# Performance work log

Measured on AMD Instinct MI355X. Metric: run time of the kernel, lower is better.

## Reference

```python
import jax, jax.numpy as jnp
import numpy as np

N, E, F_IN, H, G, A, OUT = 50000, 800000, 128, 256, 64, 8, 1


def _lin(k, fi, fo):
    s = 1.0 / np.sqrt(fi)
    kw, kb = jax.random.split(k)
    W = jax.random.uniform(kw, (fi, fo), jnp.float32, -s, s)
    b = jax.random.uniform(kb, (fo,), jnp.float32, -s, s)
    return W, b


def setup_inputs() -> dict:
    key = jax.random.key(0)
    ks = jax.random.split(key, 12)
    x = jax.random.normal(ks[0], (N, F_IN), jnp.float32)
    edge_index = jax.random.randint(ks[1], (2, E), 0, N, dtype=jnp.int64)
    batch = jnp.sort(jax.random.randint(ks[2], (N,), 0, G, dtype=jnp.int64))
    graph_attr = jax.random.normal(ks[3], (G, A), jnp.float32)
    W1, b1 = _lin(ks[4], F_IN, H)
    W2, b2 = _lin(ks[5], H, H)
    W3, b3 = _lin(ks[6], H, H)
    fcW1, fcb1 = _lin(ks[7], H + A, H)
    fcW2, fcb2 = _lin(ks[8], H, OUT)
    ones = jnp.ones((H,), jnp.float32)
    zeros = jnp.zeros((H,), jnp.float32)
    return dict(x=x, graph_attr=graph_attr, edge_index=edge_index, batch=batch,
                W1=W1, b1=b1, W2=W2, b2=b2, W3=W3, b3=b3,
                g1=ones, be1=zeros, g2=ones, be2=zeros, g3=ones, be3=zeros,
                fcW1=fcW1, fcb1=fcb1, fcW2=fcW2, fcb2=fcb2)


def gcn_conv(x, W, b, src, dst, n):
    # PyG GCNConv: add self-loops, symmetric normalization, xW then scatter-add
    xw = x @ W  # [N, H]
    loop = jnp.arange(n)
    src2 = jnp.concatenate([src, loop])
    dst2 = jnp.concatenate([dst, loop])
    deg = jnp.zeros((n,), xw.dtype).at[dst2].add(1.0)
    dinv = jnp.where(deg > 0, jax.lax.rsqrt(deg), 0.0)
    norm = dinv[src2] * dinv[dst2]  # [E+N]
    out = jnp.zeros((n, xw.shape[1]), xw.dtype).at[dst2].add(xw[src2] * norm[:, None])
    return out + b


def layer_norm(x, g, b, eps=1e-5):
    m = x.mean(-1, keepdims=True)
    v = ((x - m) ** 2).mean(-1, keepdims=True)
    return (x - m) * jax.lax.rsqrt(v + eps) * g + b


def reference(x, graph_attr, edge_index, batch,
              W1, b1, W2, b2, W3, b3,
              g1, be1, g2, be2, g3, be3,
              fcW1, fcb1, fcW2, fcb2):
    src, dst = edge_index[0], edge_index[1]
    h = jax.nn.relu(layer_norm(gcn_conv(x, W1, b1, src, dst, N), g1, be1))
    h = jax.nn.relu(layer_norm(gcn_conv(h, W2, b2, src, dst, N), g2, be2))
    h = jax.nn.relu(layer_norm(gcn_conv(h, W3, b3, src, dst, N), g3, be3))
    # global mean pool over graph ids
    sums = jax.ops.segment_sum(h, batch, num_segments=G)
    cnts = jax.ops.segment_sum(jnp.ones((N,), h.dtype), batch, num_segments=G)
    pooled = sums / jnp.maximum(cnts, 1.0)[:, None]  # [G, H]
    z = jnp.concatenate([pooled, graph_attr.reshape(-1, A)], axis=1)
    z = jax.nn.relu(z @ fcW1 + fcb1)
    return z @ fcW2 + fcb2  # [G, OUT]
```

## Files before the change

### kernel.cpp

```cpp
#include <hip/hip_runtime.h>
#include <hip/hip_bf16.h>

#define N_NODES 50000
#define N_EDGES 800000
#define F_IN    128
#define H_DIM   256
#define G_NUM   64
#define A_DIM   8

typedef __attribute__((ext_vector_type(8))) short short8v;
typedef __attribute__((ext_vector_type(4))) float float4v;
typedef __attribute__((ext_vector_type(2))) float float2v;

__device__ __forceinline__ float b2f(unsigned short u) {
    return __uint_as_float(((unsigned int)u) << 16);
}
__device__ __forceinline__ unsigned short f2b(float v) {
    return __hip_bfloat16_raw(__float2bfloat16(v)).x;
}
__device__ __forceinline__ unsigned char f2fp8(float v) {
    return (unsigned char)(__builtin_amdgcn_cvt_pk_fp8_f32(v, v, 0, false) & 0xff);
}
__device__ __forceinline__ unsigned int pack2(float a, float b) {
    return (unsigned int)f2b(a) | ((unsigned int)f2b(b) << 16);
}
__device__ __forceinline__ void accadd16(float2v* a, uint4 v) {
    a[0] += __builtin_amdgcn_cvt_pk_f32_fp8((int)v.x, false);
    a[1] += __builtin_amdgcn_cvt_pk_f32_fp8((int)v.x, true);
    a[2] += __builtin_amdgcn_cvt_pk_f32_fp8((int)v.y, false);
    a[3] += __builtin_amdgcn_cvt_pk_f32_fp8((int)v.y, true);
    a[4] += __builtin_amdgcn_cvt_pk_f32_fp8((int)v.z, false);
    a[5] += __builtin_amdgcn_cvt_pk_f32_fp8((int)v.z, true);
    a[6] += __builtin_amdgcn_cvt_pk_f32_fp8((int)v.w, false);
    a[7] += __builtin_amdgcn_cvt_pk_f32_fp8((int)v.w, true);
}

#define SK 40


__global__ __launch_bounds__(512) void fuseA_kernel(const int* __restrict__ dst,
                                                    int* __restrict__ indeg,
                                                    unsigned short* __restrict__ eloc,
                                                    const float* __restrict__ x,
                                                    const float* __restrict__ W1,
                                                    unsigned short* __restrict__ Hb,
                                                    const float* __restrict__ W2,
                                                    unsigned short* __restrict__ Wt2,
                                                    const float* __restrict__ W3,
                                                    unsigned short* __restrict__ Wt3) {
    const int EB = (N_EDGES + 511) / 512;
    const int GB = (N_NODES + 127) / 128;
    int b = blockIdx.x, t = threadIdx.x;
    if (b < EB) {
        int i = b * 512 + t;
        if (i < N_EDGES)
            eloc[i] = (unsigned short)atomicAdd(&indeg[dst[i]], 1);
        return;
    }
    b -= EB;
    if (b < GB) {
        __shared__ unsigned short As[128][SK];
        __shared__ unsigned short Bs[256][SK];
        int wave = t >> 6, lane = t & 63;
        int wm0 = (wave & 1) * 64, wn0 = (wave >> 1) * 64;
        int bm = b * 128;
        int l15 = lane & 15, lq = lane >> 4;
        float4v acc[4][4];
        #pragma unroll
        for (int i = 0; i < 4; i++)
            #pragma unroll
            for (int j = 0; j < 4; j++)
                acc[i][j] = (float4v){0.f, 0.f, 0.f, 0.f};

        for (int k0 = 0; k0 < F_IN; k0 += 32) {
            {
                int row = t >> 2, koff = (t & 3) * 8;
                short8v tmp = (short8v){0,0,0,0,0,0,0,0};
                if (bm + row < N_NODES) {
                    const float* xp = x + (size_t)(bm + row) * F_IN + k0 + koff;
                    float4 a0 = *(const float4*)xp;
                    float4 a1 = *(const float4*)(xp + 4);
                    tmp[0] = (short)f2b(a0.x); tmp[1] = (short)f2b(a0.y);
                    tmp[2] = (short)f2b(a0.z); tmp[3] = (short)f2b(a0.w);
                    tmp[4] = (short)f2b(a1.x); tmp[5] = (short)f2b(a1.y);
                    tmp[6] = (short)f2b(a1.z); tmp[7] = (short)f2b(a1.w);
                }
                *(short8v*)&As[row][koff] = tmp;
            }
            #pragma unroll
            for (int h = 0; h < 2; h++) {
                int c = t + h * 512;
                int n = c >> 2, koff = (c & 3) * 8;
                short8v tmp;
                #pragma unroll
                for (int kk = 0; kk < 8; kk++)
                    tmp[kk] = (short)f2b(W1[(size_t)(k0 + koff + kk) * H_DIM + n]);
                *(short8v*)&Bs[n][koff] = tmp;
            }
            __syncthreads();
            short8v af[4], bf[4];
            #pragma unroll
            for (int i = 0; i < 4; i++) {
                af[i] = *(const short8v*)&As[wm0 + i * 16 + l15][lq * 8];
                bf[i] = *(const short8v*)&Bs[wn0 + i * 16 + l15][lq * 8];
            }
            #pragma unroll
            for (int i = 0; i < 4; i++)
                #pragma unroll
                for (int j = 0; j < 4; j++)
                    acc[i][j] = __builtin_amdgcn_mfma_f32_16x16x32_bf16(af[i], bf[j], acc[i][j], 0, 0, 0);
            __syncthreads();
        }
        #pragma unroll
        for (int i = 0; i < 4; i++) {
            #pragma unroll
            for (int r = 0; r < 4; r++) {
                int row = bm + wm0 + i * 16 + lq * 4 + r;
                if (row < N_NODES) {
                    #pragma unroll
                    for (int j = 0; j < 4; j++) {
                        int col = wn0 + j * 16 + l15;
                        Hb[(size_t)row * H_DIM + col] = f2b(acc[i][j][r]);
                    }
                }
            }
        }
        return;
    }
    b -= GB;
    int i = b * 512 + t;
    if (i < H_DIM * H_DIM) {
        int k = i >> 8, n = i & 255;
        Wt2[(size_t)n * H_DIM + k] = f2b(W2[i]);
    } else if (i < 2 * H_DIM * H_DIM) {
        int j = i - H_DIM * H_DIM;
        int k = j >> 8, n = j & 255;
        Wt3[(size_t)n * H_DIM + k] = f2b(W3[j]);
    }
}


__global__ __launch_bounds__(256) void scan1_kernel(const int* __restrict__ in,
                                                    int* __restrict__ out,
                                                    int* __restrict__ bsum,
                                                    float* __restrict__ dinv, int n) {
    __shared__ int tile[256];
    int b = blockIdx.x, t = threadIdx.x, i = b * 256 + t;
    int v = (i < n) ? in[i] : 0;
    if (i < n) dinv[i] = rsqrtf((float)v + 1.0f);
    tile[t] = v;
    __syncthreads();
    #pragma unroll
    for (int o = 1; o < 256; o <<= 1) {
        int add = (t >= o) ? tile[t - o] : 0;
        __syncthreads();
        tile[t] += add;
        __syncthreads();
    }
    if (i < n) out[i] = tile[t] - v;
    if (t == 255) bsum[b] = tile[255];
}

__global__ __launch_bounds__(256) void scan2_kernel(int* __restrict__ bsum, int nb,
                                                    const int* __restrict__ batch,
                                                    int* __restrict__ gstart,
                                                    float* __restrict__ pooled) {
    __shared__ int tile[256];
    int t = threadIdx.x;
    int v = (t < nb) ? bsum[t] : 0;
    tile[t] = v;
    __syncthreads();
    #pragma unroll
    for (int o = 1; o < 256; o <<= 1) {
        int add = (t >= o) ? tile[t - o] : 0;
        __syncthreads();
        tile[t] += add;
        __syncthreads();
    }
    if (t < nb) bsum[t] = tile[t] - v;
    if (t <= G_NUM) {
        int lo = 0, hi = N_NODES;
        while (lo < hi) {
            int mid = (lo + hi) >> 1;
            if (batch[mid] < t) lo = mid + 1; else hi = mid;
        }
        gstart[t] = lo;
    }
    for (int i = t; i < G_NUM * H_DIM; i += 256) pooled[i] = 0.f;
}

__global__ __launch_bounds__(256) void scan3_kernel(int* __restrict__ out,
                                                    const int* __restrict__ bsum, int n) {
    int i = blockIdx.x * blockDim.x + threadIdx.x;
    if (i < n) out[i] = out[i] + bsum[i >> 8];
    if (i == 0) out[n] = N_EDGES;
}


__global__ __launch_bounds__(512) void fuseB_kernel(const int* __restrict__ src,
                                                    const int* __restrict__ dst,
                                                    const unsigned short* __restrict__ eloc,
                                                    const int* __restrict__ rowptr,
                                                    unsigned short* __restrict__ csr_src,
                                                    const uint4* __restrict__ Hb4,
                                                    const float* __restrict__ dinv,
                                                    uint2* __restrict__ P8) {
    const int PB = (N_EDGES + 511) / 512;
    int b = blockIdx.x, t = threadIdx.x;
    if (b < PB) {
        int i = b * 512 + t;
        if (i < N_EDGES) {
            int d = dst[i];
            csr_src[rowptr[d] + (int)eloc[i]] = (unsigned short)src[i];
        }
        return;
    }
    int i = (b - PB) * 512 + t;
    if (i < N_NODES * (H_DIM / 8)) {
        float dv = dinv[i >> 5];
        uint4 hv = Hb4[i];
        float f0 = b2f((unsigned short)(hv.x & 0xffffu)) * dv;
        float f1 = b2f((unsigned short)(hv.x >> 16)) * dv;
        float f2 = b2f((unsigned short)(hv.y & 0xffffu)) * dv;
        float f3 = b2f((unsigned short)(hv.y >> 16)) * dv;
        float f4 = b2f((unsigned short)(hv.z & 0xffffu)) * dv;
        float f5 = b2f((unsigned short)(hv.z >> 16)) * dv;
        float f6 = b2f((unsigned short)(hv.w & 0xffffu)) * dv;
        float f7 = b2f((unsigned short)(hv.w >> 16)) * dv;
        unsigned int lo = (unsigned int)__builtin_amdgcn_cvt_pk_fp8_f32(f0, f1, 0, false);
        lo = (unsigned int)__builtin_amdgcn_cvt_pk_fp8_f32(f2, f3, (int)lo, true);
        unsigned int hi = (unsigned int)__builtin_amdgcn_cvt_pk_fp8_f32(f4, f5, 0, false);
        hi = (unsigned int)__builtin_amdgcn_cvt_pk_fp8_f32(f6, f7, (int)hi, true);
        P8[i] = make_uint2(lo, hi);
    }
}


__device__ __forceinline__ void gemm_body_f8(const unsigned short* __restrict__ A,
                                             const unsigned short* __restrict__ Bt,
                                             unsigned char* __restrict__ C8,
                                             const float* __restrict__ dinv,
                                             int M, int K, int bm) {
    __shared__ unsigned short As[128][SK];
    __shared__ unsigned short Bs[256][SK];
    int t = threadIdx.x;
    int wave = t >> 6, lane = t & 63;
    int wm0 = (wave & 1) * 64, wn0 = (wave >> 1) * 64;
    int l15 = lane & 15, lq = lane >> 4;
    float4v acc[4][4];
    #pragma unroll
    for (int i = 0; i < 4; i++)
        #pragma unroll
        for (int j = 0; j < 4; j++)
            acc[i][j] = (float4v){0.f, 0.f, 0.f, 0.f};

    for (int k0 = 0; k0 < K; k0 += 32) {
        {
            int row = t >> 2, koff = (t & 3) * 8;
            uint4 va = make_uint4(0u, 0u, 0u, 0u);
            if (bm + row < M)
                va = *(const uint4*)(A + (size_t)(bm + row) * K + k0 + koff);
            *(uint4*)&As[row][koff] = va;
        }
        #pragma unroll
        for (int h = 0; h < 2; h++) {
            int c = t + h * 512;
            int row = c >> 2, koff = (c & 3) * 8;
            uint4 vb = *(const uint4*)(Bt + (size_t)row * K + k0 + koff);
            *(uint4*)&Bs[row][koff] = vb;
        }
        __syncthreads();
        short8v af[4], bf[4];
        #pragma unroll
        for (int i = 0; i < 4; i++) {
            af[i] = *(const short8v*)&As[wm0 + i * 16 + l15][lq * 8];
            bf[i] = *(const short8v*)&Bs[wn0 + i * 16 + l15][lq * 8];
        }
        #pragma unroll
        for (int i = 0; i < 4; i++)
            #pragma unroll
            for (int j = 0; j < 4; j++)
                acc[i][j] = __builtin_amdgcn_mfma_f32_16x16x32_bf16(af[i], bf[j], acc[i][j], 0, 0, 0);
        __syncthreads();
    }
    #pragma unroll
    for (int i = 0; i < 4; i++) {
        #pragma unroll
        for (int r = 0; r < 4; r++) {
            int row = bm + wm0 + i * 16 + lq * 4 + r;
            if (row < M) {
                float dv = dinv[row];
                #pragma unroll
                for (int j = 0; j < 4; j++) {
                    int col = wn0 + j * 16 + l15;
                    C8[(size_t)row * H_DIM + col] = f2fp8(dv * acc[i][j][r]);
                }
            }
        }
    }
}

__global__ __launch_bounds__(512) void gemm_f8(const unsigned short* __restrict__ A,
                                               const unsigned short* __restrict__ Bt,
                                               unsigned char* __restrict__ C8,
                                               const float* __restrict__ dinv,
                                               int M, int K) {
    gemm_body_f8(A, Bt, C8, dinv, M, K, blockIdx.x * 128);
}


template<int F, bool DO_LN>
__global__ __launch_bounds__(256) void gather_ns(const unsigned char* __restrict__ xw,
                                                 unsigned short* __restrict__ out,
                                                 const int* __restrict__ rowptr,
                                                 const unsigned short* __restrict__ csr_src,
                                                 const float* __restrict__ dinv,
                                                 const float* __restrict__ bias,
                                                 const float* __restrict__ gamma,
                                                 const float* __restrict__ beta) {
    constexpr int BPL = F / 16;
    constexpr int NF2 = BPL / 2;
    int lane = threadIdx.x & 63;
    int wave = threadIdx.x >> 6;
    int p = lane & 15;
    int gbase = lane & 48;
    int node = blockIdx.x * 16 + wave * 4 + (lane >> 4);
    int beg = rowptr[node];
    int deg = rowptr[node + 1] - beg;
    const unsigned char* xp = xw + (size_t)p * BPL;

    float2v acc2[NF2];
    #pragma unroll
    for (int k = 0; k < NF2; k++) acc2[k] = (float2v){0.f, 0.f};

    {
        uint4 v = *(const uint4*)(xp + (size_t)node * F);
        accadd16(acc2, v);
    }

    for (int b0 = 0; b0 < deg; b0 += 16) {
        int m = deg - b0; if (m > 16) m = 16;
        int sv = (p < m) ? (int)csr_src[beg + b0 + p] : 0;
        int j = 0;
        for (; j + 4 <= m; j += 4) {
            int s0 = __shfl(sv, gbase | j, 64);
            int s1 = __shfl(sv, gbase | (j + 1), 64);
            int s2 = __shfl(sv, gbase | (j + 2), 64);
            int s3 = __shfl(sv, gbase | (j + 3), 64);
            uint4 v0 = *(const uint4*)(xp + (size_t)s0 * F);
            uint4 v1 = *(const uint4*)(xp + (size_t)s1 * F);
            uint4 v2 = *(const uint4*)(xp + (size_t)s2 * F);
            uint4 v3 = *(const uint4*)(xp + (size_t)s3 * F);
            accadd16(acc2, v0); accadd16(acc2, v1);
            accadd16(acc2, v2); accadd16(acc2, v3);
        }
        for (; j < m; ++j) {
            int s0 = __shfl(sv, gbase | j, 64);
            uint4 v0 = *(const uint4*)(xp + (size_t)s0 * F);
            accadd16(acc2, v0);
        }
    }

    float d = dinv[node];
    float v[BPL];
    #pragma unroll
    for (int k = 0; k < NF2; k++) { v[2 * k] = d * acc2[k].x; v[2 * k + 1] = d * acc2[k].y; }

    if constexpr (DO_LN) {
        #pragma unroll
        for (int q = 0; q < BPL / 4; q++) {
            float4 bi = ((const float4*)bias)[p * (BPL / 4) + q];
            v[q * 4 + 0] += bi.x; v[q * 4 + 1] += bi.y;
            v[q * 4 + 2] += bi.z; v[q * 4 + 3] += bi.w;
        }
        float s = 0.f, ss = 0.f;
        #pragma unroll
        for (int k = 0; k < BPL; k++) { s += v[k]; ss += v[k] * v[k]; }
        #pragma unroll
        for (int o = 1; o < 16; o <<= 1) {
            s  += __shfl_xor(s, o, 64);
            ss += __shfl_xor(ss, o, 64);
        }
        float mn = s * (1.f / F);
        float var = ss * (1.f / F) - mn * mn;
        float rstd = rsqrtf(var + 1e-5f);
        #pragma unroll
        for (int q = 0; q < BPL / 4; q++) {
            float4 ga = ((const float4*)gamma)[p * (BPL / 4) + q];
            float4 be = ((const float4*)beta)[p * (BPL / 4) + q];
            v[q * 4 + 0] = fmaxf((v[q * 4 + 0] - mn) * rstd * ga.x + be.x, 0.f);
            v[q * 4 + 1] = fmaxf((v[q * 4 + 1] - mn) * rstd * ga.y + be.y, 0.f);
            v[q * 4 + 2] = fmaxf((v[q * 4 + 2] - mn) * rstd * ga.z + be.z, 0.f);
            v[q * 4 + 3] = fmaxf((v[q * 4 + 3] - mn) * rstd * ga.w + be.w, 0.f);
        }
    }

    unsigned short* op = out + (size_t)node * F + p * BPL;
    uint4 o0;
    o0.x = pack2(v[0], v[1]); o0.y = pack2(v[2], v[3]);
    o0.z = pack2(v[4], v[5]); o0.w = pack2(v[6], v[7]);
    *(uint4*)op = o0;
    if constexpr (F == 256) {
        uint4 o1;
        o1.x = pack2(v[8],  v[9]);  o1.y = pack2(v[10], v[11]);
        o1.z = pack2(v[12], v[13]); o1.w = pack2(v[14], v[15]);
        *(uint4*)(op + 8) = o1;
    }
}


__global__ __launch_bounds__(128) void pool_kernel(const unsigned int* __restrict__ h32,
                                                   const int* __restrict__ batch,
                                                   float* __restrict__ pooled, int n) {
    int t = threadIdx.x;
    int start = blockIdx.x * 64;
    int end = min(start + 64, n);
    if (start >= n) return;
    int cur = batch[start];
    float a0 = 0.f, a1 = 0.f;
    for (int i = start; i < end; ++i) {
        int g = batch[i];
        if (g != cur) {
            atomicAdd(&pooled[(size_t)cur * H_DIM + 2 * t], a0);
            atomicAdd(&pooled[(size_t)cur * H_DIM + 2 * t + 1], a1);
            a0 = a1 = 0.f;
            cur = g;
        }
        unsigned int u = h32[(size_t)i * (H_DIM / 2) + t];
        a0 += b2f((unsigned short)(u & 0xffffu));
        a1 += b2f((unsigned short)(u >> 16));
    }
    atomicAdd(&pooled[(size_t)cur * H_DIM + 2 * t], a0);
    atomicAdd(&pooled[(size_t)cur * H_DIM + 2 * t + 1], a1);
}


__global__ __launch_bounds__(256) void fc_kernel(const float* __restrict__ pooled,
                                                 const int* __restrict__ gstart,
                                                 const float* __restrict__ gattr,
                                                 const float* __restrict__ fcW1,
                                                 const float* __restrict__ fcb1,
                                                 const float* __restrict__ fcW2,
                                                 const float* __restrict__ fcb2,
                                                 float* __restrict__ out) {
    __shared__ float zc[H_DIM + A_DIM];
    __shared__ float z1[H_DIM];
    int g = blockIdx.x, t = threadIdx.x;
    int c_i = gstart[g + 1] - gstart[g];
    float c = (float)(c_i > 1 ? c_i : 1);
    zc[t] = pooled[(size_t)g * H_DIM + t] / c;
    if (t < A_DIM) zc[H_DIM + t] = gattr[g * A_DIM + t];
    __syncthreads();
    float s = fcb1[t];
    for (int k = 0; k < H_DIM + A_DIM; k++)
        s += zc[k] * fcW1[(size_t)k * H_DIM + t];
    z1[t] = fmaxf(s, 0.f) * fcW2[t];
    __syncthreads();
    for (int off = 128; off; off >>= 1) {
        if (t < off) z1[t] += z1[t + off];
        __syncthreads();
    }
    if (t == 0) out[g] = z1[0] + fcb2[0];
}


extern "C" void kernel_launch(void* const* d_in, const int* in_sizes, int n_in,
                              void* d_out, int out_size, void* d_ws, size_t ws_size,
                              hipStream_t stream) {
    const float* x     = (const float*)d_in[0];
    const float* gattr = (const float*)d_in[1];
    const int*   ei    = (const int*)d_in[2];
    const int*   batch = (const int*)d_in[3];
    const float* W1 = (const float*)d_in[4];  const float* b1 = (const float*)d_in[5];
    const float* W2 = (const float*)d_in[6];  const float* b2 = (const float*)d_in[7];
    const float* W3 = (const float*)d_in[8];  const float* b3 = (const float*)d_in[9];
    const float* g1 = (const float*)d_in[10]; const float* be1 = (const float*)d_in[11];
    const float* g2 = (const float*)d_in[12]; const float* be2 = (const float*)d_in[13];
    const float* g3 = (const float*)d_in[14]; const float* be3 = (const float*)d_in[15];
    const float* fcW1 = (const float*)d_in[16]; const float* fcb1 = (const float*)d_in[17];
    const float* fcW2 = (const float*)d_in[18]; const float* fcb2 = (const float*)d_in[19];
    float* out = (float*)d_out;

    char* w = (char*)d_ws;
    unsigned char*  Pb8 = (unsigned char*)w;  w += (size_t)N_NODES * H_DIM;
    unsigned short* Hb  = (unsigned short*)w; w += (size_t)N_NODES * H_DIM * 2;
    unsigned short* Wt2 = (unsigned short*)w; w += (size_t)H_DIM * H_DIM * 2;
    unsigned short* Wt3 = (unsigned short*)w; w += (size_t)H_DIM * H_DIM * 2;
    float* dinv   = (float*)w; w += (size_t)N_NODES * 4;
    float* pooled = (float*)w; w += (size_t)G_NUM * H_DIM * 4;
    int* indeg    = (int*)w;   w += (size_t)N_NODES * 4;
    int* rowptr   = (int*)w;   w += (size_t)(N_NODES + 4) * 4;
    unsigned short* eloc    = (unsigned short*)w; w += (size_t)N_EDGES * 2;
    unsigned short* csr_src = (unsigned short*)w; w += (size_t)N_EDGES * 2;
    int* gstart   = (int*)w;   w += (size_t)(G_NUM + 1) * 4;
    int* bsum     = (int*)w;   w += (size_t)256 * 4;

    const int* srcp = ei;
    const int* dstp = ei + N_EDGES;
    const int n_sblk = (N_NODES + 255) / 256;

    hipMemsetAsync(indeg, 0, (size_t)N_NODES * sizeof(int), stream);
    {
        const int EB = (N_EDGES + 511) / 512;
        const int GB = (N_NODES + 127) / 128;
        const int WB = (2 * H_DIM * H_DIM + 511) / 512;
        fuseA_kernel<<<EB + GB + WB, 512, 0, stream>>>(dstp, indeg, eloc, x, W1, Hb,
                                                       W2, Wt2, W3, Wt3);
    }
    scan1_kernel<<<n_sblk, 256, 0, stream>>>(indeg, rowptr, bsum, dinv, N_NODES);
    scan2_kernel<<<1, 256, 0, stream>>>(bsum, n_sblk, batch, gstart, pooled);
    scan3_kernel<<<n_sblk, 256, 0, stream>>>(rowptr, bsum, N_NODES);

    {
        const int PB = (N_EDGES + 511) / 512;
        const int RB = (N_NODES * (H_DIM / 8) + 511) / 512;
        fuseB_kernel<<<PB + RB, 512, 0, stream>>>(srcp, dstp, eloc, rowptr, csr_src,
                                                  (const uint4*)Hb, dinv, (uint2*)Pb8);
    }

    int gemm_blocks = (N_NODES + 127) / 128;
    int gather_blocks = N_NODES / 16;

    gather_ns<H_DIM, true><<<gather_blocks, 256, 0, stream>>>(Pb8, Hb, rowptr, csr_src, dinv,
                                                              b1, g1, be1);
    gemm_f8<<<gemm_blocks, 512, 0, stream>>>(Hb, Wt2, Pb8, dinv, N_NODES, H_DIM);
    gather_ns<H_DIM, true><<<gather_blocks, 256, 0, stream>>>(Pb8, Hb, rowptr, csr_src, dinv,
                                                              b2, g2, be2);
    gemm_f8<<<gemm_blocks, 512, 0, stream>>>(Hb, Wt3, Pb8, dinv, N_NODES, H_DIM);
    gather_ns<H_DIM, true><<<gather_blocks, 256, 0, stream>>>(Pb8, Hb, rowptr, csr_src, dinv,
                                                              b3, g3, be3);

    pool_kernel<<<(N_NODES + 63) / 64, 128, 0, stream>>>((const unsigned int*)Hb, batch, pooled, N_NODES);
    fc_kernel<<<G_NUM, 256, 0, stream>>>(pooled, gstart, gattr, fcW1, fcb1, fcW2, fcb2, out);
}
```

Before: 373.9 us.

## Build CSR via bucketed two-level counting sort and fold dinv into first gather

Replaces the global-atomic in-degree count, three-pass scan and scatter with a two-level counting sort. Edges are binned into 256-node buckets using per-chunk LDS histograms. Each bucket is then sorted in LDS to produce rowptr, dinv and csr_src. The first GEMM now writes fp8 directly, without source-side dinv scaling, so the separate bf16-to-fp8 rescale pass is removed. The first gather applies the per-neighbor dinv weight in an FMA instead. This trades global atomics and extra passes for more kernels and an extra per-edge dinv load in layer one, and edge order within a row changes.

```diff
diff --git a/kernel.cpp b/kernel.cpp
--- a/kernel.cpp
+++ b/kernel.cpp
@@ -7,6 +7,11 @@
 #define H_DIM   256
 #define G_NUM   64
 #define A_DIM   8
+
+#define NBUCKET 196
+#define NCHUNK  391
+#define CHUNK   2048
+#define K4CAP   6144
 
 typedef __attribute__((ext_vector_type(8))) short short8v;
 typedef __attribute__((ext_vector_type(4))) float float4v;
@@ -34,30 +39,48 @@
     a[6] += __builtin_amdgcn_cvt_pk_f32_fp8((int)v.w, false);
     a[7] += __builtin_amdgcn_cvt_pk_f32_fp8((int)v.w, true);
 }
+__device__ __forceinline__ void accfma16(float2v* a, uint4 v, float w) {
+    float2v w2 = {w, w};
+    a[0] = __builtin_amdgcn_cvt_pk_f32_fp8((int)v.x, false) * w2 + a[0];
+    a[1] = __builtin_amdgcn_cvt_pk_f32_fp8((int)v.x, true)  * w2 + a[1];
+    a[2] = __builtin_amdgcn_cvt_pk_f32_fp8((int)v.y, false) * w2 + a[2];
+    a[3] = __builtin_amdgcn_cvt_pk_f32_fp8((int)v.y, true)  * w2 + a[3];
+    a[4] = __builtin_amdgcn_cvt_pk_f32_fp8((int)v.z, false) * w2 + a[4];
+    a[5] = __builtin_amdgcn_cvt_pk_f32_fp8((int)v.z, true)  * w2 + a[5];
+    a[6] = __builtin_amdgcn_cvt_pk_f32_fp8((int)v.w, false) * w2 + a[6];
+    a[7] = __builtin_amdgcn_cvt_pk_f32_fp8((int)v.w, true)  * w2 + a[7];
+}
 
 #define SK 40
 
 
-__global__ __launch_bounds__(512) void fuseA_kernel(const int* __restrict__ dst,
-                                                    int* __restrict__ indeg,
-                                                    unsigned short* __restrict__ eloc,
+__global__ __launch_bounds__(512) void fuse0_kernel(const int* __restrict__ dst,
+                                                    unsigned int* __restrict__ Hg,
                                                     const float* __restrict__ x,
                                                     const float* __restrict__ W1,
-                                                    unsigned short* __restrict__ Hb,
+                                                    unsigned char* __restrict__ P8,
                                                     const float* __restrict__ W2,
                                                     unsigned short* __restrict__ Wt2,
                                                     const float* __restrict__ W3,
                                                     unsigned short* __restrict__ Wt3) {
-    const int EB = (N_EDGES + 511) / 512;
+    const int CB = NCHUNK;
     const int GB = (N_NODES + 127) / 128;
     int b = blockIdx.x, t = threadIdx.x;
-    if (b < EB) {
-        int i = b * 512 + t;
-        if (i < N_EDGES)
-            eloc[i] = (unsigned short)atomicAdd(&indeg[dst[i]], 1);
+    if (b < CB) {
+        __shared__ unsigned int h[256];
+        if (t < 256) h[t] = 0u;
+        __syncthreads();
+        int base = b * CHUNK;
+        #pragma unroll
+        for (int k = 0; k < 4; k++) {
+            int i = base + k * 512 + t;
+            if (i < N_EDGES) atomicAdd(&h[dst[i] >> 8], 1u);
+        }
+        __syncthreads();
+        if (t < 256) Hg[(size_t)t * NCHUNK + b] = h[t];
         return;
     }
-    b -= EB;
+    b -= CB;
     if (b < GB) {
         __shared__ unsigned short As[128][SK];
         __shared__ unsigned short Bs[256][SK];
@@ -120,7 +143,7 @@
                     #pragma unroll
                     for (int j = 0; j < 4; j++) {
                         int col = wn0 + j * 16 + l15;
-                        Hb[(size_t)row * H_DIM + col] = f2b(acc[i][j][r]);
+                        P8[(size_t)row * H_DIM + col] = f2fp8(acc[i][j][r]);
                     }
                 }
             }
@@ -140,44 +163,52 @@
 }
 
 
-__global__ __launch_bounds__(256) void scan1_kernel(const int* __restrict__ in,
-                                                    int* __restrict__ out,
-                                                    int* __restrict__ bsum,
-                                                    float* __restrict__ dinv, int n) {
-    __shared__ int tile[256];
-    int b = blockIdx.x, t = threadIdx.x, i = b * 256 + t;
-    int v = (i < n) ? in[i] : 0;
-    if (i < n) dinv[i] = rsqrtf((float)v + 1.0f);
+__global__ __launch_bounds__(256) void scanH_kernel(unsigned int* __restrict__ Hg,
+                                                    unsigned int* __restrict__ Btot) {
+    __shared__ unsigned int tile[256];
+    int b = blockIdx.x, t = threadIdx.x;
+    unsigned int* row = Hg + (size_t)b * NCHUNK;
+    int i0 = 2 * t, i1 = 2 * t + 1;
+    unsigned int v0 = (i0 < NCHUNK) ? row[i0] : 0u;
+    unsigned int v1 = (i1 < NCHUNK) ? row[i1] : 0u;
+    unsigned int pair = v0 + v1;
+    tile[t] = pair;
+    __syncthreads();
+    #pragma unroll
+    for (int o = 1; o < 256; o <<= 1) {
+        unsigned int add = (t >= o) ? tile[t - o] : 0u;
+        __syncthreads();
+        tile[t] += add;
+        __syncthreads();
+    }
+    unsigned int excl = tile[t] - pair;
+    if (i0 < NCHUNK) row[i0] = excl;
+    if (i1 < NCHUNK) row[i1] = excl + v0;
+    if (t == 255) Btot[b] = tile[255];
+}
+
+
+__global__ __launch_bounds__(256) void base_kernel(const unsigned int* __restrict__ Btot,
+                                                   unsigned int* __restrict__ bucketBase,
+                                                   const int* __restrict__ batch,
+                                                   int* __restrict__ gstart,
+                                                   int* __restrict__ rowptr,
+                                                   float* __restrict__ pooled) {
+    __shared__ unsigned int tile[256];
+    int t = threadIdx.x;
+    unsigned int v = (t < NBUCKET) ? Btot[t] : 0u;
     tile[t] = v;
     __syncthreads();
     #pragma unroll
     for (int o = 1; o < 256; o <<= 1) {
-        int add = (t >= o) ? tile[t - o] : 0;
+        unsigned int add = (t >= o) ? tile[t - o] : 0u;
         __syncthreads();
         tile[t] += add;
         __syncthreads();
     }
-    if (i < n) out[i] = tile[t] - v;
-    if (t == 255) bsum[b] = tile[255];
-}
-
-__global__ __launch_bounds__(256) void scan2_kernel(int* __restrict__ bsum, int nb,
-                                                    const int* __restrict__ batch,
-                                                    int* __restrict__ gstart,
-                                                    float* __restrict__ pooled) {
-    __shared__ int tile[256];
-    int t = threadIdx.x;
-    int v = (t < nb) ? bsum[t] : 0;
-    tile[t] = v;
-    __syncthreads();
-    #pragma unroll
-    for (int o = 1; o < 256; o <<= 1) {
-        int add = (t >= o) ? tile[t - o] : 0;
-        __syncthreads();
-        tile[t] += add;
-        __syncthreads();
-    }
-    if (t < nb) bsum[t] = tile[t] - v;
+    if (t < NBUCKET) bucketBase[t] = tile[t] - v;
+    if (t == NBUCKET - 1) bucketBase[NBUCKET] = tile[t];
+    if (t == 0) rowptr[N_NODES] = N_EDGES;
     if (t <= G_NUM) {
         int lo = 0, hi = N_NODES;
         while (lo < hi) {
@@ -189,63 +220,89 @@
     for (int i = t; i < G_NUM * H_DIM; i += 256) pooled[i] = 0.f;
 }
 
-__global__ __launch_bounds__(256) void scan3_kernel(int* __restrict__ out,
-                                                    const int* __restrict__ bsum, int n) {
-    int i = blockIdx.x * blockDim.x + threadIdx.x;
-    if (i < n) out[i] = out[i] + bsum[i >> 8];
-    if (i == 0) out[n] = N_EDGES;
-}
-
-
-__global__ __launch_bounds__(512) void fuseB_kernel(const int* __restrict__ src,
-                                                    const int* __restrict__ dst,
-                                                    const unsigned short* __restrict__ eloc,
-                                                    const int* __restrict__ rowptr,
-                                                    unsigned short* __restrict__ csr_src,
-                                                    const uint4* __restrict__ Hb4,
-                                                    const float* __restrict__ dinv,
-                                                    uint2* __restrict__ P8) {
-    const int PB = (N_EDGES + 511) / 512;
+
+__global__ __launch_bounds__(512) void scatter_kernel(const int* __restrict__ src,
+                                                      const int* __restrict__ dst,
+                                                      const unsigned int* __restrict__ Hg,
+                                                      const unsigned int* __restrict__ bucketBase,
+                                                      unsigned int* __restrict__ tmp) {
+    __shared__ unsigned int off[256];
+    int blk = blockIdx.x, t = threadIdx.x;
+    if (t < 256)
+        off[t] = (t < NBUCKET) ? (bucketBase[t] + Hg[(size_t)t * NCHUNK + blk]) : 0u;
+    __syncthreads();
+    int base = blk * CHUNK;
+    #pragma unroll
+    for (int k = 0; k < 4; k++) {
+        int i = base + k * 512 + t;
+        if (i < N_EDGES) {
+            int d = dst[i], s = src[i];
+            unsigned int slot = atomicAdd(&off[d >> 8], 1u);
+            tmp[slot] = ((unsigned int)(d & 255) << 16) | (unsigned int)s;
+        }
+    }
+}
+
+
+__global__ __launch_bounds__(256) void finalize_kernel(const unsigned int* __restrict__ tmp,
+                                                       const unsigned int* __restrict__ bucketBase,
+                                                       int* __restrict__ rowptr,
+                                                       float* __restrict__ dinv,
+                                                       unsigned short* __restrict__ csr_src) {
+    __shared__ unsigned int te[K4CAP];
+    __shared__ unsigned int h2[256];
+    __shared__ unsigned int sc[256];
+    __shared__ unsigned int off2[256];
     int b = blockIdx.x, t = threadIdx.x;
-    if (b < PB) {
-        int i = b * 512 + t;
-        if (i < N_EDGES) {
-            int d = dst[i];
-            csr_src[rowptr[d] + (int)eloc[i]] = (unsigned short)src[i];
-        }
-        return;
-    }
-    int i = (b - PB) * 512 + t;
-    if (i < N_NODES * (H_DIM / 8)) {
-        float dv = dinv[i >> 5];
-        uint4 hv = Hb4[i];
-        float f0 = b2f((unsigned short)(hv.x & 0xffffu)) * dv;
-        float f1 = b2f((unsigned short)(hv.x >> 16)) * dv;
-        float f2 = b2f((unsigned short)(hv.y & 0xffffu)) * dv;
-        float f3 = b2f((unsigned short)(hv.y >> 16)) * dv;
-        float f4 = b2f((unsigned short)(hv.z & 0xffffu)) * dv;
-        float f5 = b2f((unsigned short)(hv.z >> 16)) * dv;
-        float f6 = b2f((unsigned short)(hv.w & 0xffffu)) * dv;
-        float f7 = b2f((unsigned short)(hv.w >> 16)) * dv;
-        unsigned int lo = (unsigned int)__builtin_amdgcn_cvt_pk_fp8_f32(f0, f1, 0, false);
-        lo = (unsigned int)__builtin_amdgcn_cvt_pk_fp8_f32(f2, f3, (int)lo, true);
-        unsigned int hi = (unsigned int)__builtin_amdgcn_cvt_pk_fp8_f32(f4, f5, 0, false);
-        hi = (unsigned int)__builtin_amdgcn_cvt_pk_fp8_f32(f6, f7, (int)hi, true);
-        P8[i] = make_uint2(lo, hi);
-    }
-}
-
-
-__device__ __forceinline__ void gemm_body_f8(const unsigned short* __restrict__ A,
-                                             const unsigned short* __restrict__ Bt,
-                                             unsigned char* __restrict__ C8,
-                                             const float* __restrict__ dinv,
-                                             int M, int K, int bm) {
+    unsigned int beg = bucketBase[b], end = bucketBase[b + 1];
+    int cnt = (int)(end - beg);
+    bool lds_ok = (cnt <= K4CAP);
+    h2[t] = 0u;
+    __syncthreads();
+    for (int i = t; i < cnt; i += 256) {
+        unsigned int u = tmp[beg + i];
+        if (lds_ok) te[i] = u;
+        atomicAdd(&h2[u >> 16], 1u);
+    }
+    __syncthreads();
+    unsigned int c = h2[t];
+    sc[t] = c;
+    __syncthreads();
+    #pragma unroll
+    for (int o = 1; o < 256; o <<= 1) {
+        unsigned int add = (t >= o) ? sc[t - o] : 0u;
+        __syncthreads();
+        sc[t] += add;
+        __syncthreads();
+    }
+    unsigned int excl = sc[t] - c;
+    int v = (b << 8) + t;
+    if (v < N_NODES) {
+        rowptr[v] = (int)(beg + excl);
+        dinv[v] = rsqrtf((float)c + 1.0f);
+    }
+    off2[t] = excl;
+    __syncthreads();
+    for (int i = t; i < cnt; i += 256) {
+        unsigned int u = lds_ok ? te[i] : tmp[beg + i];
+        unsigned int lo = u >> 16;
+        unsigned int s2 = atomicAdd(&off2[lo], 1u);
+        csr_src[beg + s2] = (unsigned short)(u & 0xFFFFu);
+    }
+}
+
+
+__global__ __launch_bounds__(512) void gemm_f8(const unsigned short* __restrict__ A,
+                                               const unsigned short* __restrict__ Bt,
+                                               unsigned char* __restrict__ C8,
+                                               const float* __restrict__ dinv,
+                                               int M, int K) {
     __shared__ unsigned short As[128][SK];
     __shared__ unsigned short Bs[256][SK];
     int t = threadIdx.x;
     int wave = t >> 6, lane = t & 63;
     int wm0 = (wave & 1) * 64, wn0 = (wave >> 1) * 64;
+    int bm = blockIdx.x * 128;
     int l15 = lane & 15, lq = lane >> 4;
     float4v acc[4][4];
     #pragma unroll
@@ -300,16 +357,8 @@
     }
 }
 
-__global__ __launch_bounds__(512) void gemm_f8(const unsigned short* __restrict__ A,
-                                               const unsigned short* __restrict__ Bt,
-                                               unsigned char* __restrict__ C8,
-                                               const float* __restrict__ dinv,
-                                               int M, int K) {
-    gemm_body_f8(A, Bt, C8, dinv, M, K, blockIdx.x * 128);
-}
-
-
-template<int F, bool DO_LN>
+
+template<int F, bool DO_LN, bool W8>
 __global__ __launch_bounds__(256) void gather_ns(const unsigned char* __restrict__ xw,
                                                  unsigned short* __restrict__ out,
                                                  const int* __restrict__ rowptr,
@@ -327,6 +376,7 @@
     int node = blockIdx.x * 16 + wave * 4 + (lane >> 4);
     int beg = rowptr[node];
     int deg = rowptr[node + 1] - beg;
+    float d = dinv[node];
     const unsigned char* xp = xw + (size_t)p * BPL;
 
     float2v acc2[NF2];
@@ -335,12 +385,17 @@
 
     {
         uint4 v = *(const uint4*)(xp + (size_t)node * F);
-        accadd16(acc2, v);
+        if constexpr (W8) accfma16(acc2, v, d);
+        else              accadd16(acc2, v);
     }
 
     for (int b0 = 0; b0 < deg; b0 += 16) {
         int m = deg - b0; if (m > 16) m = 16;
-        int sv = (p < m) ? (int)csr_src[beg + b0 + p] : 0;
+        int sv = 0; float wv = 0.f;
+        if (p < m) {
+            sv = (int)csr_src[beg + b0 + p];
+            if constexpr (W8) wv = dinv[sv];
+        }
         int j = 0;
         for (; j + 4 <= m; j += 4) {
             int s0 = __shfl(sv, gbase | j, 64);
@@ -351,17 +406,30 @@
             uint4 v1 = *(const uint4*)(xp + (size_t)s1 * F);
             uint4 v2 = *(const uint4*)(xp + (size_t)s2 * F);
             uint4 v3 = *(const uint4*)(xp + (size_t)s3 * F);
-            accadd16(acc2, v0); accadd16(acc2, v1);
-            accadd16(acc2, v2); accadd16(acc2, v3);
+            if constexpr (W8) {
+                float w0 = __shfl(wv, gbase | j, 64);
+                float w1 = __shfl(wv, gbase | (j + 1), 64);
+                float w2 = __shfl(wv, gbase | (j + 2), 64);
+                float w3 = __shfl(wv, gbase | (j + 3), 64);
+                accfma16(acc2, v0, w0); accfma16(acc2, v1, w1);
+                accfma16(acc2, v2, w2); accfma16(acc2, v3, w3);
+            } else {
+                accadd16(acc2, v0); accadd16(acc2, v1);
+                accadd16(acc2, v2); accadd16(acc2, v3);
+            }
         }
         for (; j < m; ++j) {
             int s0 = __shfl(sv, gbase | j, 64);
             uint4 v0 = *(const uint4*)(xp + (size_t)s0 * F);
-            accadd16(acc2, v0);
-        }
-    }
-
-    float d = dinv[node];
+            if constexpr (W8) {
+                float w0 = __shfl(wv, gbase | j, 64);
+                accfma16(acc2, v0, w0);
+            } else {
+                accadd16(acc2, v0);
+            }
+        }
+    }
+
     float v[BPL];
     #pragma unroll
     for (int k = 0; k < NF2; k++) { v[2 * k] = d * acc2[k].x; v[2 * k + 1] = d * acc2[k].y; }
@@ -488,47 +556,39 @@
     unsigned short* Wt3 = (unsigned short*)w; w += (size_t)H_DIM * H_DIM * 2;
     float* dinv   = (float*)w; w += (size_t)N_NODES * 4;
     float* pooled = (float*)w; w += (size_t)G_NUM * H_DIM * 4;
-    int* indeg    = (int*)w;   w += (size_t)N_NODES * 4;
     int* rowptr   = (int*)w;   w += (size_t)(N_NODES + 4) * 4;
-    unsigned short* eloc    = (unsigned short*)w; w += (size_t)N_EDGES * 2;
+    unsigned int* Hg = (unsigned int*)w;      w += (size_t)256 * NCHUNK * 4;
+    unsigned int* Btot = (unsigned int*)w;    w += (size_t)256 * 4;
+    unsigned int* bucketBase = (unsigned int*)w; w += (size_t)(NBUCKET + 4) * 4;
+    unsigned int* tmp = (unsigned int*)w;     w += (size_t)N_EDGES * 4;
     unsigned short* csr_src = (unsigned short*)w; w += (size_t)N_EDGES * 2;
     int* gstart   = (int*)w;   w += (size_t)(G_NUM + 1) * 4;
-    int* bsum     = (int*)w;   w += (size_t)256 * 4;
 
     const int* srcp = ei;
     const int* dstp = ei + N_EDGES;
-    const int n_sblk = (N_NODES + 255) / 256;
-
-    hipMemsetAsync(indeg, 0, (size_t)N_NODES * sizeof(int), stream);
+
     {
-        const int EB = (N_EDGES + 511) / 512;
+        const int CB = NCHUNK;
         const int GB = (N_NODES + 127) / 128;
         const int WB = (2 * H_DIM * H_DIM + 511) / 512;
-        fuseA_kernel<<<EB + GB + WB, 512, 0, stream>>>(dstp, indeg, eloc, x, W1, Hb,
-                                                       W2, Wt2, W3, Wt3);
-    }
-    scan1_kernel<<<n_sblk, 256, 0, stream>>>(indeg, rowptr, bsum, dinv, N_NODES);
-    scan2_kernel<<<1, 256, 0, stream>>>(bsum, n_sblk, batch, gstart, pooled);
-    scan3_kernel<<<n_sblk, 256, 0, stream>>>(rowptr, bsum, N_NODES);
-
-    {
-        const int PB = (N_EDGES + 511) / 512;
-        const int RB = (N_NODES * (H_DIM / 8) + 511) / 512;
-        fuseB_kernel<<<PB + RB, 512, 0, stream>>>(srcp, dstp, eloc, rowptr, csr_src,
-                                                  (const uint4*)Hb, dinv, (uint2*)Pb8);
-    }
+        fuse0_kernel<<<CB + GB + WB, 512, 0, stream>>>(dstp, Hg, x, W1, Pb8, W2, Wt2, W3, Wt3);
+    }
+    scanH_kernel<<<NBUCKET, 256, 0, stream>>>(Hg, Btot);
+    base_kernel<<<1, 256, 0, stream>>>(Btot, bucketBase, batch, gstart, rowptr, pooled);
+    scatter_kernel<<<NCHUNK, 512, 0, stream>>>(srcp, dstp, Hg, bucketBase, tmp);
+    finalize_kernel<<<NBUCKET, 256, 0, stream>>>(tmp, bucketBase, rowptr, dinv, csr_src);
 
     int gemm_blocks = (N_NODES + 127) / 128;
     int gather_blocks = N_NODES / 16;
 
-    gather_ns<H_DIM, true><<<gather_blocks, 256, 0, stream>>>(Pb8, Hb, rowptr, csr_src, dinv,
-                                                              b1, g1, be1);
+    gather_ns<H_DIM, true, true><<<gather_blocks, 256, 0, stream>>>(Pb8, Hb, rowptr, csr_src,
+                                                                    dinv, b1, g1, be1);
     gemm_f8<<<gemm_blocks, 512, 0, stream>>>(Hb, Wt2, Pb8, dinv, N_NODES, H_DIM);
-    gather_ns<H_DIM, true><<<gather_blocks, 256, 0, stream>>>(Pb8, Hb, rowptr, csr_src, dinv,
-                                                              b2, g2, be2);
+    gather_ns<H_DIM, true, false><<<gather_blocks, 256, 0, stream>>>(Pb8, Hb, rowptr, csr_src,
+                                                                     dinv, b2, g2, be2);
     gemm_f8<<<gemm_blocks, 512, 0, stream>>>(Hb, Wt3, Pb8, dinv, N_NODES, H_DIM);
-    gather_ns<H_DIM, true><<<gather_blocks, 256, 0, stream>>>(Pb8, Hb, rowptr, csr_src, dinv,
-                                                              b3, g3, be3);
+    gather_ns<H_DIM, true, false><<<gather_blocks, 256, 0, stream>>>(Pb8, Hb, rowptr, csr_src,
+                                                                     dinv, b3, g3, be3);
 
     pool_kernel<<<(N_NODES + 63) / 64, 128, 0, stream>>>((const unsigned int*)Hb, batch, pooled, N_NODES);
     fc_kernel<<<G_NUM, 256, 0, stream>>>(pooled, gstart, gattr, fcW1, fcb1, fcW2, fcb2, out);
```

Measured after the change: 339.3 us. 9.3% less time.
